# Performance work log

Hardware: AMD Instinct MI355X
Metric: run time of the kernel (lower is better)

## Reference

```python
import jax, jax.numpy as jnp
import numpy as np

# Dims: L list entries, T hutch samples, D = output_dim*inducing_size, H = 16 hidden
L, T, D, H = 32, 64, 8192, 16


def setup_inputs() -> dict:
    key = jax.random.key(0)
    k = jax.random.split(key, 4)
    return {
        "u": jax.random.normal(k[0], (L, D), jnp.float32),
        "w": jax.random.normal(k[1], (L, T, D), jnp.float32),  # Hutchinson Gaussian probes
        "W1": jax.random.normal(k[2], (H, D), jnp.float32) / np.sqrt(D).astype(np.float32),
        "b1": jnp.zeros((H,), jnp.float32),
        "W2": jax.random.normal(k[3], (D, H), jnp.float32) / np.sqrt(H).astype(np.float32),
        "b2": jnp.zeros((D,), jnp.float32),
    }


def reference(u, w, W1, b1, W2, b2):
    # f = W2 tanh(W1 u + b1) + b2 ; Jacobian J = W2 diag(1 - h^2) W1
    h = jnp.tanh(u @ W1.T + b1)                 # [L, H]
    f = h @ W2.T + b2                           # [L, D]  (f_u_list stacked)
    s = 1.0 - h * h                             # tanh' at preactivation, [L, H]
    # u_grad = J^T w  computed without materializing J: W1^T diag(s) W2^T w
    v = jnp.einsum('ltd,dh->lth', w, W2)        # W2^T w, [L, T, H]
    v = v * s[:, None, :]                       # diag(s) applied
    g = jnp.einsum('lth,hd->ltd', v, W1)        # J^T w, [L, T, D]
    traces = jnp.sum(g * w, axis=-1)            # w^T J w, [L, T]
    # mean over hutch samples, then mean over list entries -> [1, 1] like torch.mm output
    trace_final_mean = jnp.mean(traces).reshape(1, 1)
    return f, trace_final_mean
```

## Files before the change

### kernel.cpp

```cpp
#include <hip/hip_runtime.h>

typedef __attribute__((ext_vector_type(8))) short bf16x8;
typedef __attribute__((ext_vector_type(4))) float f32x4;

namespace {
constexpr int L = 32, T = 64, D = 8192, H = 16;
constexpr int M = L * T;
constexpr int KP = 64;
constexpr int CHUNK = D / KP;

constexpr size_t WS_WH  = 0;
constexpr size_t WS_WL  = WS_WH + 32 * 8192 / 2;
constexpr size_t WS_PRE = WS_WL + 32 * 8192 / 2;
constexpr size_t WS_AC  = WS_PRE + 32 * 8 * 16;
}

__device__ inline void split1(float f, short& h, short& l) {
  unsigned b = __float_as_uint(f);
  h = (short)(b >> 16);
  float lf = f - __uint_as_float(b & 0xFFFF0000u);
  l = (short)(__float_as_uint(lf) >> 16);
}

__device__ inline void split8(float4 a0, float4 a1, bf16x8& h, bf16x8& l) {
  float f[8] = {a0.x, a0.y, a0.z, a0.w, a1.x, a1.y, a1.z, a1.w};
#pragma unroll
  for (int i = 0; i < 8; ++i) {
    short hh, ll;
    split1(f[i], hh, ll);
    h[i] = hh; l[i] = ll;
  }
}

__global__ __launch_bounds__(256) void k_setup(
    const float* __restrict__ u, const float* __restrict__ W1,
    const float* __restrict__ W2,
    ushort* __restrict__ wh, ushort* __restrict__ wl,
    float* __restrict__ pre, float* __restrict__ ac,
    float* __restrict__ out) {
  int b = blockIdx.x, tid = threadIdx.x;
  if (b == 0 && tid == 0) out[(size_t)L * D] = 0.f;
  if (b < 32) {
    int d = b * 256 + tid;
    const float4* src = reinterpret_cast<const float4*>(W2 + (size_t)d * 16);
    float4 q0 = src[0], q1 = src[1], q2 = src[2], q3 = src[3];
    float v[16] = {q0.x, q0.y, q0.z, q0.w, q1.x, q1.y, q1.z, q1.w,
                   q2.x, q2.y, q2.z, q2.w, q3.x, q3.y, q3.z, q3.w};
#pragma unroll
    for (int c = 0; c < 16; ++c) {
      short hh, ll;
      split1(v[c], hh, ll);
      wh[(size_t)c * D + d] = (ushort)hh;
      wl[(size_t)c * D + d] = (ushort)ll;
    }
  } else if (b < 64) {
    int q = (b - 32) * 256 + tid;
#pragma unroll
    for (int j = 0; j < 4; ++j) {
      int idx = (q + j * 8192) * 4;
      float4 qv = *reinterpret_cast<const float4*>(W1 + idx);
      short h0, l0, h1, l1, h2, l2, h3, l3;
      split1(qv.x, h0, l0); split1(qv.y, h1, l1);
      split1(qv.z, h2, l2); split1(qv.w, h3, l3);
      ushort4 vh = {(ushort)h0, (ushort)h1, (ushort)h2, (ushort)h3};
      ushort4 vl = {(ushort)l0, (ushort)l1, (ushort)l2, (ushort)l3};
      *reinterpret_cast<ushort4*>(wh + (size_t)16 * D + idx) = vh;
      *reinterpret_cast<ushort4*>(wl + (size_t)16 * D + idx) = vl;
    }
  } else if (b < 80) {
    int t = (b - 64) * 256 + tid;
    float4 z = {0.f, 0.f, 0.f, 0.f};
    float4* dst = reinterpret_cast<float4*>(ac);
#pragma unroll
    for (int j = 0; j < 4; ++j) dst[t + j * 4096] = z;
  } else {
    int bb = b - 80;
    int kc = bb & 7, l = bb >> 3;
    int d = kc * 1024 + tid * 4;
    float4 uv = *reinterpret_cast<const float4*>(u + (size_t)l * D + d);
    float acc[16];
#pragma unroll
    for (int h = 0; h < 16; ++h) {
      float4 wv = *reinterpret_cast<const float4*>(W1 + (size_t)h * D + d);
      float t = fmaf(uv.x, wv.x, 0.f);
      t = fmaf(uv.y, wv.y, t);
      t = fmaf(uv.z, wv.z, t);
      acc[h] = fmaf(uv.w, wv.w, t);
    }
#pragma unroll
    for (int h = 0; h < 16; ++h)
      for (int off = 1; off < 64; off <<= 1) acc[h] += __shfl_xor(acc[h], off);
    __shared__ float red[4][16];
    int lane = tid & 63, wv_ = tid >> 6;
    if (lane == 0) {
#pragma unroll
      for (int h = 0; h < 16; ++h) red[wv_][h] = acc[h];
    }
    __syncthreads();
    if (tid < 16)
      pre[((size_t)l * 8 + kc) * 16 + tid] =
          red[0][tid] + red[1][tid] + red[2][tid] + red[3][tid];
  }
}

__global__ __launch_bounds__(256, 8) void k_trace_ac(
    const float* __restrict__ w,
    const ushort* __restrict__ wh, const ushort* __restrict__ wl,
    float* __restrict__ ac) {
  int tid = threadIdx.x;
  int wave = tid >> 6, lane = tid & 63;
  int lrow = lane & 15, kg = lane >> 4;
  int kp = blockIdx.x;
  int rt = blockIdx.y * 4 + wave;
  int m0 = rt * 16;
  int k0 = kp * CHUNK;

  const float*  wrow = w  + (size_t)(m0 + lrow) * D + k0 + kg * 8;
  const ushort* bh0  = wh + (size_t)lrow * D + k0 + kg * 8;
  const ushort* bl0  = wl + (size_t)lrow * D + k0 + kg * 8;
  const ushort* bh1  = bh0 + (size_t)16 * D;
  const ushort* bl1  = bl0 + (size_t)16 * D;

  f32x4 acc0 = {0.f, 0.f, 0.f, 0.f};
  f32x4 acc1 = {0.f, 0.f, 0.f, 0.f};

#pragma unroll
  for (int kk = 0; kk < CHUNK / 32; ++kk) {
    int off = kk * 32;
    float4 a0 = *reinterpret_cast<const float4*>(wrow + off);
    float4 a1 = *reinterpret_cast<const float4*>(wrow + off + 4);
    bf16x8 ah, al;
    split8(a0, a1, ah, al);
    bf16x8 vbh0 = *reinterpret_cast<const bf16x8*>(bh0 + off);
    bf16x8 vbl0 = *reinterpret_cast<const bf16x8*>(bl0 + off);
    bf16x8 vbh1 = *reinterpret_cast<const bf16x8*>(bh1 + off);
    bf16x8 vbl1 = *reinterpret_cast<const bf16x8*>(bl1 + off);
    acc0 = __builtin_amdgcn_mfma_f32_16x16x32_bf16(ah, vbh0, acc0, 0, 0, 0);
    acc0 = __builtin_amdgcn_mfma_f32_16x16x32_bf16(ah, vbl0, acc0, 0, 0, 0);
    acc0 = __builtin_amdgcn_mfma_f32_16x16x32_bf16(al, vbh0, acc0, 0, 0, 0);
    acc1 = __builtin_amdgcn_mfma_f32_16x16x32_bf16(ah, vbh1, acc1, 0, 0, 0);
    acc1 = __builtin_amdgcn_mfma_f32_16x16x32_bf16(ah, vbl1, acc1, 0, 0, 0);
    acc1 = __builtin_amdgcn_mfma_f32_16x16x32_bf16(al, vbh1, acc1, 0, 0, 0);
  }

  float* dst = ac + (size_t)(m0 + kg * 4) * 32;
#pragma unroll
  for (int j = 0; j < 4; ++j) {
    atomicAdd(dst + (size_t)j * 32 + lrow,      acc0[j]);
    atomicAdd(dst + (size_t)j * 32 + 16 + lrow, acc1[j]);
  }
}

__global__ __launch_bounds__(256) void k_tail(
    const float* __restrict__ pre, const float* __restrict__ b1,
    const float* __restrict__ W2, const float* __restrict__ b2,
    const float* __restrict__ ac, float* __restrict__ out) {
  __shared__ float hl[8][16];
  __shared__ float s[16];
  __shared__ float red[4];
  int b = blockIdx.x, tid = threadIdx.x;
  if (b >= 128) {
    int bb = b - 128;
    int l = bb >> 3;
    if (tid < 16) {
      float p = b1[tid];
#pragma unroll
      for (int kc = 0; kc < 8; ++kc) p += pre[((size_t)l * 8 + kc) * 16 + tid];
      float t = tanhf(p);
      s[tid] = 1.f - t * t;
    }
    __syncthreads();
    int c = tid & 31;
    float acc = ac[(size_t)bb * 256 + tid];
    float partner = __shfl_xor(acc, 16);
    float t = (c < 16) ? s[c] * acc * partner : 0.f;
#pragma unroll
    for (int off = 1; off < 64; off <<= 1) t += __shfl_xor(t, off);
    int lane = tid & 63, wv_ = tid >> 6;
    if (lane == 0) red[wv_] = t;
    __syncthreads();
    if (tid == 0)
      atomicAdd(out + (size_t)L * D,
                (red[0] + red[1] + red[2] + red[3]) * (1.0f / (float)(L * T)));
    return;
  }
  int lg = b >> 5;
  if (tid < 128) {
    int ll = tid >> 4, h = tid & 15, l = lg * 8 + ll;
    float p = b1[h];
#pragma unroll
    for (int kc = 0; kc < 8; ++kc) p += pre[((size_t)l * 8 + kc) * 16 + h];
    hl[ll][h] = tanhf(p);
  }
  __syncthreads();
  int d = (b & 31) * 256 + tid;
  const float4* w2r = reinterpret_cast<const float4*>(W2 + (size_t)d * 16);
  float4 q0 = w2r[0], q1 = w2r[1], q2 = w2r[2], q3 = w2r[3];
  float w2v[16] = {q0.x, q0.y, q0.z, q0.w, q1.x, q1.y, q1.z, q1.w,
                   q2.x, q2.y, q2.z, q2.w, q3.x, q3.y, q3.z, q3.w};
  float bv = b2[d];
#pragma unroll
  for (int ll = 0; ll < 8; ++ll) {
    float fv = bv;
#pragma unroll
    for (int h = 0; h < 16; ++h) fv = fmaf(hl[ll][h], w2v[h], fv);
    out[(size_t)(lg * 8 + ll) * D + d] = fv;
  }
}

extern "C" void kernel_launch(void* const* d_in, const int* in_sizes, int n_in,
                              void* d_out, int out_size, void* d_ws, size_t ws_size,
                              hipStream_t stream) {
  const float* u  = (const float*)d_in[0];
  const float* w  = (const float*)d_in[1];
  const float* W1 = (const float*)d_in[2];
  const float* b1 = (const float*)d_in[3];
  const float* W2 = (const float*)d_in[4];
  const float* b2 = (const float*)d_in[5];
  float* out = (float*)d_out;
  float* ws  = (float*)d_ws;
  ushort* wcat_h = (ushort*)(ws + WS_WH);
  ushort* wcat_l = (ushort*)(ws + WS_WL);
  float* pre = ws + WS_PRE;
  float* acb = ws + WS_AC;

  hipLaunchKernelGGL(k_setup,    dim3(336), dim3(256), 0, stream,
                     u, W1, W2, wcat_h, wcat_l, pre, acb, out);
  hipLaunchKernelGGL(k_trace_ac, dim3(KP, 32), dim3(256), 0, stream,
                     w, wcat_h, wcat_l, acb);
  hipLaunchKernelGGL(k_tail,     dim3(384), dim3(256), 0, stream,
                     pre, b1, W2, b2, acb, out);
}
```

Measured before the change: 128.8 us.

## Fuse setup, trace GEMM and tail into one cooperative kernel with grid syncs

Replaces three kernel launches with a single cooperative kernel of 1024 blocks that uses grid.sync between the setup, MFMA trace-accumulation and tail phases. KP is halved so each block handles a longer K chunk and the grid size matches 1024 blocks, which also halves the number of atomic adds into the accumulator. This removes inter-kernel launch gaps, but adds grid-wide barrier cost and lowers occupancy (launch bounds now 4 blocks per SM) for the memory-bound GEMM phase.

```diff
diff --git a/kernel.cpp b/kernel.cpp
--- a/kernel.cpp
+++ b/kernel.cpp
@@ -1,4 +1,7 @@
 #include <hip/hip_runtime.h>
+#include <hip/hip_cooperative_groups.h>
+
+namespace cg = cooperative_groups;
 
 typedef __attribute__((ext_vector_type(8))) short bf16x8;
 typedef __attribute__((ext_vector_type(4))) float f32x4;
@@ -6,7 +9,7 @@
 namespace {
 constexpr int L = 32, T = 64, D = 8192, H = 16;
 constexpr int M = L * T;
-constexpr int KP = 64;
+constexpr int KP = 32;
 constexpr int CHUNK = D / KP;
 
 constexpr size_t WS_WH  = 0;
@@ -32,13 +35,21 @@
   }
 }
 
-__global__ __launch_bounds__(256) void k_setup(
-    const float* __restrict__ u, const float* __restrict__ W1,
-    const float* __restrict__ W2,
+__global__ __launch_bounds__(256, 4) void k_fused(
+    const float* __restrict__ u, const float* __restrict__ w,
+    const float* __restrict__ W1, const float* __restrict__ b1,
+    const float* __restrict__ W2, const float* __restrict__ b2,
     ushort* __restrict__ wh, ushort* __restrict__ wl,
     float* __restrict__ pre, float* __restrict__ ac,
     float* __restrict__ out) {
-  int b = blockIdx.x, tid = threadIdx.x;
+  cg::grid_group grid = cg::this_grid();
+  __shared__ float redA[4][16];
+  __shared__ float hl[8][16];
+  __shared__ float s[16];
+  __shared__ float redC[4];
+
+  const int b = blockIdx.x, tid = threadIdx.x;
+
   if (b == 0 && tid == 0) out[(size_t)L * D] = 0.f;
   if (b < 32) {
     int d = b * 256 + tid;
@@ -73,7 +84,7 @@
     float4* dst = reinterpret_cast<float4*>(ac);
 #pragma unroll
     for (int j = 0; j < 4; ++j) dst[t + j * 4096] = z;
-  } else {
+  } else if (b < 336) {
     int bb = b - 80;
     int kc = bb & 7, l = bb >> 3;
     int d = kc * 1024 + tid * 4;
@@ -90,76 +101,89 @@
 #pragma unroll
     for (int h = 0; h < 16; ++h)
       for (int off = 1; off < 64; off <<= 1) acc[h] += __shfl_xor(acc[h], off);
-    __shared__ float red[4][16];
     int lane = tid & 63, wv_ = tid >> 6;
     if (lane == 0) {
 #pragma unroll
-      for (int h = 0; h < 16; ++h) red[wv_][h] = acc[h];
+      for (int h = 0; h < 16; ++h) redA[wv_][h] = acc[h];
     }
     __syncthreads();
     if (tid < 16)
       pre[((size_t)l * 8 + kc) * 16 + tid] =
-          red[0][tid] + red[1][tid] + red[2][tid] + red[3][tid];
-  }
-}
-
-__global__ __launch_bounds__(256, 8) void k_trace_ac(
-    const float* __restrict__ w,
-    const ushort* __restrict__ wh, const ushort* __restrict__ wl,
-    float* __restrict__ ac) {
-  int tid = threadIdx.x;
-  int wave = tid >> 6, lane = tid & 63;
-  int lrow = lane & 15, kg = lane >> 4;
-  int kp = blockIdx.x;
-  int rt = blockIdx.y * 4 + wave;
-  int m0 = rt * 16;
-  int k0 = kp * CHUNK;
-
-  const float*  wrow = w  + (size_t)(m0 + lrow) * D + k0 + kg * 8;
-  const ushort* bh0  = wh + (size_t)lrow * D + k0 + kg * 8;
-  const ushort* bl0  = wl + (size_t)lrow * D + k0 + kg * 8;
-  const ushort* bh1  = bh0 + (size_t)16 * D;
-  const ushort* bl1  = bl0 + (size_t)16 * D;
-
-  f32x4 acc0 = {0.f, 0.f, 0.f, 0.f};
-  f32x4 acc1 = {0.f, 0.f, 0.f, 0.f};
-
-#pragma unroll
-  for (int kk = 0; kk < CHUNK / 32; ++kk) {
-    int off = kk * 32;
-    float4 a0 = *reinterpret_cast<const float4*>(wrow + off);
-    float4 a1 = *reinterpret_cast<const float4*>(wrow + off + 4);
-    bf16x8 ah, al;
-    split8(a0, a1, ah, al);
-    bf16x8 vbh0 = *reinterpret_cast<const bf16x8*>(bh0 + off);
-    bf16x8 vbl0 = *reinterpret_cast<const bf16x8*>(bl0 + off);
-    bf16x8 vbh1 = *reinterpret_cast<const bf16x8*>(bh1 + off);
-    bf16x8 vbl1 = *reinterpret_cast<const bf16x8*>(bl1 + off);
-    acc0 = __builtin_amdgcn_mfma_f32_16x16x32_bf16(ah, vbh0, acc0, 0, 0, 0);
-    acc0 = __builtin_amdgcn_mfma_f32_16x16x32_bf16(ah, vbl0, acc0, 0, 0, 0);
-    acc0 = __builtin_amdgcn_mfma_f32_16x16x32_bf16(al, vbh0, acc0, 0, 0, 0);
-    acc1 = __builtin_amdgcn_mfma_f32_16x16x32_bf16(ah, vbh1, acc1, 0, 0, 0);
-    acc1 = __builtin_amdgcn_mfma_f32_16x16x32_bf16(ah, vbl1, acc1, 0, 0, 0);
-    acc1 = __builtin_amdgcn_mfma_f32_16x16x32_bf16(al, vbh1, acc1, 0, 0, 0);
-  }
-
-  float* dst = ac + (size_t)(m0 + kg * 4) * 32;
-#pragma unroll
-  for (int j = 0; j < 4; ++j) {
-    atomicAdd(dst + (size_t)j * 32 + lrow,      acc0[j]);
-    atomicAdd(dst + (size_t)j * 32 + 16 + lrow, acc1[j]);
-  }
-}
-
-__global__ __launch_bounds__(256) void k_tail(
-    const float* __restrict__ pre, const float* __restrict__ b1,
-    const float* __restrict__ W2, const float* __restrict__ b2,
-    const float* __restrict__ ac, float* __restrict__ out) {
-  __shared__ float hl[8][16];
-  __shared__ float s[16];
-  __shared__ float red[4];
-  int b = blockIdx.x, tid = threadIdx.x;
-  if (b >= 128) {
+          redA[0][tid] + redA[1][tid] + redA[2][tid] + redA[3][tid];
+  }
+
+  grid.sync();
+
+  {
+    int wave = tid >> 6, lane = tid & 63;
+    int lrow = lane & 15, kg = lane >> 4;
+    int kp = b & 31;
+    int rt = (b >> 5) * 4 + wave;
+    int m0 = rt * 16;
+    int k0 = kp * CHUNK;
+
+    const float*  wrow = w  + (size_t)(m0 + lrow) * D + k0 + kg * 8;
+    const ushort* bh0  = wh + (size_t)lrow * D + k0 + kg * 8;
+    const ushort* bl0  = wl + (size_t)lrow * D + k0 + kg * 8;
+    const ushort* bh1  = bh0 + (size_t)16 * D;
+    const ushort* bl1  = bl0 + (size_t)16 * D;
+
+    f32x4 acc0 = {0.f, 0.f, 0.f, 0.f};
+    f32x4 acc1 = {0.f, 0.f, 0.f, 0.f};
+
+#pragma unroll
+    for (int kk = 0; kk < CHUNK / 32; ++kk) {
+      int off = kk * 32;
+      float4 a0 = *reinterpret_cast<const float4*>(wrow + off);
+      float4 a1 = *reinterpret_cast<const float4*>(wrow + off + 4);
+      bf16x8 ah, al;
+      split8(a0, a1, ah, al);
+      bf16x8 vbh0 = *reinterpret_cast<const bf16x8*>(bh0 + off);
+      bf16x8 vbl0 = *reinterpret_cast<const bf16x8*>(bl0 + off);
+      bf16x8 vbh1 = *reinterpret_cast<const bf16x8*>(bh1 + off);
+      bf16x8 vbl1 = *reinterpret_cast<const bf16x8*>(bl1 + off);
+      acc0 = __builtin_amdgcn_mfma_f32_16x16x32_bf16(ah, vbh0, acc0, 0, 0, 0);
+      acc0 = __builtin_amdgcn_mfma_f32_16x16x32_bf16(ah, vbl0, acc0, 0, 0, 0);
+      acc0 = __builtin_amdgcn_mfma_f32_16x16x32_bf16(al, vbh0, acc0, 0, 0, 0);
+      acc1 = __builtin_amdgcn_mfma_f32_16x16x32_bf16(ah, vbh1, acc1, 0, 0, 0);
+      acc1 = __builtin_amdgcn_mfma_f32_16x16x32_bf16(ah, vbl1, acc1, 0, 0, 0);
+      acc1 = __builtin_amdgcn_mfma_f32_16x16x32_bf16(al, vbh1, acc1, 0, 0, 0);
+    }
+
+    float* dst = ac + (size_t)(m0 + kg * 4) * 32;
+#pragma unroll
+    for (int j = 0; j < 4; ++j) {
+      atomicAdd(dst + (size_t)j * 32 + lrow,      acc0[j]);
+      atomicAdd(dst + (size_t)j * 32 + 16 + lrow, acc1[j]);
+    }
+  }
+
+  grid.sync();
+
+  if (b < 128) {
+    int lg = b >> 5;
+    if (tid < 128) {
+      int ll = tid >> 4, h = tid & 15, l = lg * 8 + ll;
+      float p = b1[h];
+#pragma unroll
+      for (int kc = 0; kc < 8; ++kc) p += pre[((size_t)l * 8 + kc) * 16 + h];
+      hl[ll][h] = tanhf(p);
+    }
+    __syncthreads();
+    int d = (b & 31) * 256 + tid;
+    const float4* w2r = reinterpret_cast<const float4*>(W2 + (size_t)d * 16);
+    float4 q0 = w2r[0], q1 = w2r[1], q2 = w2r[2], q3 = w2r[3];
+    float w2v[16] = {q0.x, q0.y, q0.z, q0.w, q1.x, q1.y, q1.z, q1.w,
+                     q2.x, q2.y, q2.z, q2.w, q3.x, q3.y, q3.z, q3.w};
+    float bv = b2[d];
+#pragma unroll
+    for (int ll = 0; ll < 8; ++ll) {
+      float fv = bv;
+#pragma unroll
+      for (int h = 0; h < 16; ++h) fv = fmaf(hl[ll][h], w2v[h], fv);
+      out[(size_t)(lg * 8 + ll) * D + d] = fv;
+    }
+  } else if (b < 384) {
     int bb = b - 128;
     int l = bb >> 3;
     if (tid < 16) {
@@ -177,34 +201,11 @@
 #pragma unroll
     for (int off = 1; off < 64; off <<= 1) t += __shfl_xor(t, off);
     int lane = tid & 63, wv_ = tid >> 6;
-    if (lane == 0) red[wv_] = t;
+    if (lane == 0) redC[wv_] = t;
     __syncthreads();
     if (tid == 0)
       atomicAdd(out + (size_t)L * D,
-                (red[0] + red[1] + red[2] + red[3]) * (1.0f / (float)(L * T)));
-    return;
-  }
-  int lg = b >> 5;
-  if (tid < 128) {
-    int ll = tid >> 4, h = tid & 15, l = lg * 8 + ll;
-    float p = b1[h];
-#pragma unroll
-    for (int kc = 0; kc < 8; ++kc) p += pre[((size_t)l * 8 + kc) * 16 + h];
-    hl[ll][h] = tanhf(p);
-  }
-  __syncthreads();
-  int d = (b & 31) * 256 + tid;
-  const float4* w2r = reinterpret_cast<const float4*>(W2 + (size_t)d * 16);
-  float4 q0 = w2r[0], q1 = w2r[1], q2 = w2r[2], q3 = w2r[3];
-  float w2v[16] = {q0.x, q0.y, q0.z, q0.w, q1.x, q1.y, q1.z, q1.w,
-                   q2.x, q2.y, q2.z, q2.w, q3.x, q3.y, q3.z, q3.w};
-  float bv = b2[d];
-#pragma unroll
-  for (int ll = 0; ll < 8; ++ll) {
-    float fv = bv;
-#pragma unroll
-    for (int h = 0; h < 16; ++h) fv = fmaf(hl[ll][h], w2v[h], fv);
-    out[(size_t)(lg * 8 + ll) * D + d] = fv;
+                (redC[0] + redC[1] + redC[2] + redC[3]) * (1.0f / (float)(L * T)));
   }
 }
 
@@ -224,10 +225,9 @@
   float* pre = ws + WS_PRE;
   float* acb = ws + WS_AC;
 
-  hipLaunchKernelGGL(k_setup,    dim3(336), dim3(256), 0, stream,
-                     u, W1, W2, wcat_h, wcat_l, pre, acb, out);
-  hipLaunchKernelGGL(k_trace_ac, dim3(KP, 32), dim3(256), 0, stream,
-                     w, wcat_h, wcat_l, acb);
-  hipLaunchKernelGGL(k_tail,     dim3(384), dim3(256), 0, stream,
-                     pre, b1, W2, b2, acb, out);
-}
+  void* args[] = {(void*)&u, (void*)&w, (void*)&W1, (void*)&b1, (void*)&W2,
+                  (void*)&b2, (void*)&wcat_h, (void*)&wcat_l, (void*)&pre,
+                  (void*)&acb, (void*)&out};
+  hipLaunchCooperativeKernel((const void*)k_fused, dim3(1024), dim3(256),
+                             args, 0, stream);
+}
```

After: 372.7 us. 189% more time.

## Halve K-split blocks, drop occupancy hint, and software-prefetch next k-step operands

Applied to the files above, without the earlier changes.

Halves the number of K-partitions in the trace kernel so each block processes a longer chunk (16 instead of 8 k-steps), cutting the number of atomicAdd partial sums written to the accumulator. Removes the 8-blocks-per-CU launch bound, letting the compiler use more registers. Adds explicit register double-buffering that loads the next step's w and weight fragments before issuing the current MFMAs. Fewer blocks (1024) and possibly more register pressure may reduce occupancy and latency hiding for this memory-bound stream over w.

```diff
diff --git a/kernel.cpp b/kernel.cpp
--- a/kernel.cpp
+++ b/kernel.cpp
@@ -6,7 +6,7 @@
 namespace {
 constexpr int L = 32, T = 64, D = 8192, H = 16;
 constexpr int M = L * T;
-constexpr int KP = 64;
+constexpr int KP = 32;
 constexpr int CHUNK = D / KP;
 
 constexpr size_t WS_WH  = 0;
@@ -103,7 +103,7 @@
   }
 }
 
-__global__ __launch_bounds__(256, 8) void k_trace_ac(
+__global__ __launch_bounds__(256) void k_trace_ac(
     const float* __restrict__ w,
     const ushort* __restrict__ wh, const ushort* __restrict__ wl,
     float* __restrict__ ac) {
@@ -124,23 +124,38 @@
   f32x4 acc0 = {0.f, 0.f, 0.f, 0.f};
   f32x4 acc1 = {0.f, 0.f, 0.f, 0.f};
 
+  float4 a0 = *reinterpret_cast<const float4*>(wrow);
+  float4 a1 = *reinterpret_cast<const float4*>(wrow + 4);
+  bf16x8 vbh0 = *reinterpret_cast<const bf16x8*>(bh0);
+  bf16x8 vbl0 = *reinterpret_cast<const bf16x8*>(bl0);
+  bf16x8 vbh1 = *reinterpret_cast<const bf16x8*>(bh1);
+  bf16x8 vbl1 = *reinterpret_cast<const bf16x8*>(bl1);
+
 #pragma unroll
   for (int kk = 0; kk < CHUNK / 32; ++kk) {
-    int off = kk * 32;
-    float4 a0 = *reinterpret_cast<const float4*>(wrow + off);
-    float4 a1 = *reinterpret_cast<const float4*>(wrow + off + 4);
+    float4 na0, na1;
+    bf16x8 nbh0, nbl0, nbh1, nbl1;
+    if (kk + 1 < CHUNK / 32) {
+      int noff = (kk + 1) * 32;
+      na0  = *reinterpret_cast<const float4*>(wrow + noff);
+      na1  = *reinterpret_cast<const float4*>(wrow + noff + 4);
+      nbh0 = *reinterpret_cast<const bf16x8*>(bh0 + noff);
+      nbl0 = *reinterpret_cast<const bf16x8*>(bl0 + noff);
+      nbh1 = *reinterpret_cast<const bf16x8*>(bh1 + noff);
+      nbl1 = *reinterpret_cast<const bf16x8*>(bl1 + noff);
+    }
     bf16x8 ah, al;
     split8(a0, a1, ah, al);
-    bf16x8 vbh0 = *reinterpret_cast<const bf16x8*>(bh0 + off);
-    bf16x8 vbl0 = *reinterpret_cast<const bf16x8*>(bl0 + off);
-    bf16x8 vbh1 = *reinterpret_cast<const bf16x8*>(bh1 + off);
-    bf16x8 vbl1 = *reinterpret_cast<const bf16x8*>(bl1 + off);
     acc0 = __builtin_amdgcn_mfma_f32_16x16x32_bf16(ah, vbh0, acc0, 0, 0, 0);
     acc0 = __builtin_amdgcn_mfma_f32_16x16x32_bf16(ah, vbl0, acc0, 0, 0, 0);
     acc0 = __builtin_amdgcn_mfma_f32_16x16x32_bf16(al, vbh0, acc0, 0, 0, 0);
     acc1 = __builtin_amdgcn_mfma_f32_16x16x32_bf16(ah, vbh1, acc1, 0, 0, 0);
     acc1 = __builtin_amdgcn_mfma_f32_16x16x32_bf16(ah, vbl1, acc1, 0, 0, 0);
     acc1 = __builtin_amdgcn_mfma_f32_16x16x32_bf16(al, vbh1, acc1, 0, 0, 0);
+    if (kk + 1 < CHUNK / 32) {
+      a0 = na0; a1 = na1;
+      vbh0 = nbh0; vbl0 = nbl0; vbh1 = nbh1; vbl1 = nbl1;
+    }
   }
 
   float* dst = ac + (size_t)(m0 + kg * 4) * 32;
```

Measured after the change: 127.7 us. Within noise of the previous version (-0.8%).
